# Performance work log

Measured on AMD Instinct MI355X. Metric: run time of the kernel, lower is better.

## Reference

```python
import jax, jax.numpy as jnp
import numpy as np

BN_EPS = 1e-5
LEAKY_SLOPE = 0.2


def setup_inputs() -> dict:
    key = jax.random.key(0)
    k1, k2 = jax.random.split(key, 2)
    B, C, N, O, K = 8, 64, 4096, 64, 20
    x = jax.random.normal(k1, (B, C, N), dtype=jnp.float32)
    W = jax.random.normal(k2, (O, 2 * C), dtype=jnp.float32) * 0.05  # 1x1 conv weight
    gamma = jnp.ones((O,), dtype=jnp.float32)
    beta = jnp.zeros((O,), dtype=jnp.float32)
    return {"x": x, "W": W, "gamma": gamma, "beta": beta, "k": K}


def reference(x, W, gamma, beta, k):
    # x: (B, C, N)
    xt = jnp.transpose(x, (0, 2, 1))  # (B, N, C)
    # kNN via squared euclidean distances (same ordering as cdist p=2)
    sq = jnp.sum(xt * xt, axis=-1)  # (B, N)
    d2 = sq[:, :, None] + sq[:, None, :] - 2.0 * jnp.einsum('bnc,bmc->bnm', xt, xt)
    idx = jax.lax.top_k(-d2, k)[1]  # (B, N, k) nearest neighbors (incl. self)
    # gather neighbor features: (B, N, k, C)
    xj = jax.vmap(lambda f, i: f[i])(xt, idx)
    xi = xt[:, :, None, :]  # (B, N, 1, C)
    edge = jnp.concatenate([xj - xi, jnp.broadcast_to(xi, xj.shape)], axis=-1)  # (B, N, k, 2C)
    # 1x1 conv == channel GEMM
    h = jnp.einsum('bnkc,oc->bnko', edge, W)  # (B, N, k, O)
    # BatchNorm2d, training-mode batch statistics over (B, N, k) per channel
    mean = jnp.mean(h, axis=(0, 1, 2))
    var = jnp.mean(jnp.square(h - mean), axis=(0, 1, 2))
    hn = (h - mean) * jax.lax.rsqrt(var + BN_EPS) * gamma + beta
    # LeakyReLU(0.2); dropout omitted (eval / identity)
    act = jnp.where(hn >= 0, hn, LEAKY_SLOPE * hn)
    # max over the k neighbors -> (B, N, O) -> (B, O, N)
    out = jnp.max(act, axis=2)
    return jnp.transpose(out, (0, 2, 1))
```

## Files before the change

### kernel.cpp

```cpp
#include <hip/hip_runtime.h>
#include <math.h>

#define Bn 8
#define Cc 64
#define Nn 4096
#define Oo 64
#define Kk 20
#define Kh 10
#define QCAP 16
#define NTOT (Bn*Nn*Kk)

typedef __attribute__((ext_vector_type(8))) short short8;
typedef __attribute__((ext_vector_type(4))) float f32x4;

__device__ __forceinline__ unsigned bf16_rn(float v) {
  unsigned u = __float_as_uint(v);
  return (u + 0x7FFFu + ((u >> 16) & 1)) >> 16;
}

__global__ __launch_bounds__(256) void k_split(const float* __restrict__ x,
                                               unsigned short* __restrict__ xs3,
                                               float* __restrict__ sqv) {
  __shared__ float xs[64][68];
  int tid = threadIdx.x;
  int b = blockIdx.x & 7;
  int n0 = (blockIdx.x >> 3) << 6;
  for (int i = 0; i < 4; i++) {
    int c = i * 16 + (tid >> 4);
    int n = (tid & 15) * 4;
    float4 v = *(const float4*)&x[((size_t)b * Cc + c) * Nn + n0 + n];
    *(float4*)&xs[c][n] = v;
  }
  __syncthreads();
  for (int i = 0; i < 4; i++) {
    int n = i * 16 + (tid >> 4);
    int c = (tid & 15) * 4;
    ushort4 h4, m4, l4;
    unsigned short* hp = (unsigned short*)&h4;
    unsigned short* mp = (unsigned short*)&m4;
    unsigned short* lp = (unsigned short*)&l4;
#pragma unroll
    for (int j = 0; j < 4; j++) {
      float v = xs[c + j][n];
      unsigned hb = bf16_rn(v);
      float hf = __uint_as_float(hb << 16);
      float r1 = v - hf;
      unsigned mb = bf16_rn(r1);
      float mf = __uint_as_float(mb << 16);
      float r2 = r1 - mf;
      unsigned lb = bf16_rn(r2);
      hp[j] = (unsigned short)hb;
      mp[j] = (unsigned short)mb;
      lp[j] = (unsigned short)lb;
    }
    size_t o = ((size_t)(b << 12) + n0 + n) * 192 + c;
    *(ushort4*)&xs3[o] = h4;
    *(ushort4*)&xs3[o + 64] = m4;
    *(ushort4*)&xs3[o + 128] = l4;
  }
  if (tid < 64) {
    float s = 0.f;
#pragma unroll
    for (int c = 0; c < 64; c++) { float v = xs[c][tid]; s = fmaf(v, v, s); }
    sqv[b * Nn + n0 + tid] = s;
  }
}

__global__ __launch_bounds__(256) void k_y1z(const float* __restrict__ x,
                                             const float* __restrict__ Wm,
                                             float* __restrict__ y1,
                                             float* __restrict__ z) {
  __shared__ float xs[64][68];
  __shared__ float Wl[64][129];
  int tid = threadIdx.x;
  int b = blockIdx.x & 7;
  int n0 = (blockIdx.x >> 3) << 6;
  for (int i = tid; i < 64 * 128; i += 256) Wl[i >> 7][i & 127] = Wm[i];
  for (int i = 0; i < 4; i++) {
    int c = i * 16 + (tid >> 4);
    int n = (tid & 15) * 4;
    float4 v = *(const float4*)&x[((size_t)b * Cc + c) * Nn + n0 + n];
    *(float4*)&xs[c][n] = v;
  }
  __syncthreads();
  int o = tid & 63, ng = tid >> 6;
  for (int p = 0; p < 4; p++) {
    int nb = p * 16 + ng * 4;
    float a1[4] = {0.f, 0.f, 0.f, 0.f};
    float a2[4] = {0.f, 0.f, 0.f, 0.f};
#pragma unroll 8
    for (int c = 0; c < 64; c++) {
      float4 xv = *(const float4*)&xs[c][nb];
      float w1v = Wl[o][c], w2v = Wl[o][64 + c];
      float xa[4] = {xv.x, xv.y, xv.z, xv.w};
#pragma unroll
      for (int j = 0; j < 4; j++) {
        a1[j] = fmaf(xa[j], w1v, a1[j]);
        a2[j] = fmaf(xa[j], w2v, a2[j]);
      }
    }
#pragma unroll
    for (int j = 0; j < 4; j++) {
      size_t off = ((size_t)b * Nn + n0 + nb + j) * 64 + o;
      y1[off] = a1[j];
      z[off] = a2[j] - a1[j];
    }
  }
}

__global__ __launch_bounds__(256, 4) void k_knn(const unsigned short* __restrict__ xs3,
                                                const float* __restrict__ sqv,
                                                int* __restrict__ idxout) {
  __shared__ alignas(16) short Bs[3][64][72];
  __shared__ float thrS[64];
  __shared__ float sqs[64];
  __shared__ alignas(16) float qk[64][20];
  __shared__ alignas(16) unsigned short qm[64][24];
  __shared__ int qcnt[64];

  const int tid = threadIdx.x;
  const int lane = tid & 63;
  const int w = tid >> 6;
  const int b = blockIdx.x & 7;
  const int n0 = (blockIdx.x >> 3) << 6;
  const int lm = lane & 15;
  const int q = lane >> 4;
  const bool handler = (lane < 32);
  const int hrow = w * 16 + (lane >> 1);
  const bool isL = (lane & 1) == 0;

  float hk[Kh];
  int hix[Kh];
#pragma unroll
  for (int kk = 0; kk < Kh; kk++) { hk[kk] = INFINITY; hix[kk] = 0; }

  if (handler && !isL) { thrS[hrow] = INFINITY; qcnt[hrow] = 0; }

  const size_t arow = ((size_t)(b << 12) + n0 + w * 16 + lm) * 192;
  short8 ah0 = *(const short8*)&xs3[arow + q * 8];
  short8 ah1 = *(const short8*)&xs3[arow + 32 + q * 8];
  short8 am0 = *(const short8*)&xs3[arow + 64 + q * 8];
  short8 am1 = *(const short8*)&xs3[arow + 96 + q * 8];
  short8 al0 = *(const short8*)&xs3[arow + 128 + q * 8];
  short8 al1 = *(const short8*)&xs3[arow + 160 + q * 8];

  const unsigned short* gp = xs3 + (size_t)(b << 12) * 192 + tid * 8;
  short* ld[6];
#pragma unroll
  for (int i = 0; i < 6; i++) {
    int f = i * 256 + tid;
    int r = f / 24;
    int rem = f - r * 24;
    int layer = rem >> 3;
    int qq = rem & 7;
    ld[i] = &Bs[layer][r][qq * 8];
  }

  f32x4 acc[4];

  for (int m0 = 0; m0 < Nn; m0 += 64) {
    __syncthreads();
#pragma unroll
    for (int i = 0; i < 6; i++) {
      short8 v = *(const short8*)(gp + i * 2048);
      *(short8*)ld[i] = v;
    }
    gp += 12288;
    if (tid < 16) ((float4*)sqs)[tid] = ((const float4*)(sqv + b * Nn + m0))[tid];
    __syncthreads();

#pragma unroll
    for (int g = 0; g < 4; g++) {
      const int mr = g * 16 + lm;
      short8 bh0 = *(const short8*)&Bs[0][mr][q * 8];
      short8 bh1 = *(const short8*)&Bs[0][mr][32 + q * 8];
      short8 bm0 = *(const short8*)&Bs[1][mr][q * 8];
      short8 bm1 = *(const short8*)&Bs[1][mr][32 + q * 8];
      short8 bl0 = *(const short8*)&Bs[2][mr][q * 8];
      short8 bl1 = *(const short8*)&Bs[2][mr][32 + q * 8];
      f32x4 a = (f32x4){0.f, 0.f, 0.f, 0.f};
      a = __builtin_amdgcn_mfma_f32_16x16x32_bf16(am0, bm0, a, 0, 0, 0);
      a = __builtin_amdgcn_mfma_f32_16x16x32_bf16(am1, bm1, a, 0, 0, 0);
      a = __builtin_amdgcn_mfma_f32_16x16x32_bf16(ah0, bl0, a, 0, 0, 0);
      a = __builtin_amdgcn_mfma_f32_16x16x32_bf16(ah1, bl1, a, 0, 0, 0);
      a = __builtin_amdgcn_mfma_f32_16x16x32_bf16(al0, bh0, a, 0, 0, 0);
      a = __builtin_amdgcn_mfma_f32_16x16x32_bf16(al1, bh1, a, 0, 0, 0);
      a = __builtin_amdgcn_mfma_f32_16x16x32_bf16(ah0, bm0, a, 0, 0, 0);
      a = __builtin_amdgcn_mfma_f32_16x16x32_bf16(ah1, bm1, a, 0, 0, 0);
      a = __builtin_amdgcn_mfma_f32_16x16x32_bf16(am0, bh0, a, 0, 0, 0);
      a = __builtin_amdgcn_mfma_f32_16x16x32_bf16(am1, bh1, a, 0, 0, 0);
      a = __builtin_amdgcn_mfma_f32_16x16x32_bf16(ah0, bh0, a, 0, 0, 0);
      a = __builtin_amdgcn_mfma_f32_16x16x32_bf16(ah1, bh1, a, 0, 0, 0);
      acc[g] = a;
    }

    unsigned pend = 0;
    {
      float tl[4];
#pragma unroll
      for (int r = 0; r < 4; r++) tl[r] = thrS[w * 16 + q * 4 + r];
#pragma unroll
      for (int g = 0; g < 4; g++) {
        float sv = sqs[g * 16 + lm];
#pragma unroll
        for (int r = 0; r < 4; r++) {
          float key = fmaf(-2.f, acc[g][r], sv);
          acc[g][r] = key;
          if (key < tl[r]) pend |= 1u << (g * 4 + r);
        }
      }
    }

    for (;;) {
      if (pend) {
#pragma unroll
        for (int g = 0; g < 4; g++) {
#pragma unroll
          for (int r = 0; r < 4; r++) {
            unsigned bit = 1u << (g * 4 + r);
            if (pend & bit) {
              int row = w * 16 + q * 4 + r;
              int p = atomicAdd(&qcnt[row], 1);
              if (p < QCAP) {
                qk[row][p] = acc[g][r];
                qm[row][p] = (unsigned short)(m0 + g * 16 + lm);
                pend &= ~bit;
              }
            }
          }
        }
      }
      unsigned long long anyovf = __ballot(pend != 0);

      if (handler) {
        int cn = qcnt[hrow];
        if (cn > QCAP) cn = QCAP;
        for (int p0 = 0; p0 < cn; p0 += 4) {
          float4 kv4 = *(const float4*)&qk[hrow][p0];
          ushort4 mv4 = *(const ushort4*)&qm[hrow][p0];
          float kva[4] = {kv4.x, kv4.y, kv4.z, kv4.w};
          unsigned short mva[4] = {mv4.x, mv4.y, mv4.z, mv4.w};
#pragma unroll
          for (int j = 0; j < 4; j++) {
            bool valid = (p0 + j < cn);
            float kv = kva[j];
            int ki = (int)mva[j];
            bool lins = kv < hk[Kh - 1];
            float pv = lins ? hk[Kh - 1] : kv;
            int pi = lins ? hix[Kh - 1] : ki;
            float rv = __shfl_xor(pv, 1);
            int ri = __shfl_xor(pi, 1);
            float mval = isL ? kv : rv;
            int midx = isL ? ki : ri;
            if (valid && mval < hk[Kh - 1]) {
              bool cm[Kh];
#pragma unroll
              for (int kk = 0; kk < Kh; kk++) cm[kk] = mval < hk[kk];
#pragma unroll
              for (int kk = Kh - 1; kk >= 1; kk--) {
                hk[kk]  = cm[kk] ? (cm[kk - 1] ? hk[kk - 1]  : mval) : hk[kk];
                hix[kk] = cm[kk] ? (cm[kk - 1] ? hix[kk - 1] : midx) : hix[kk];
              }
              if (cm[0]) { hk[0] = mval; hix[0] = midx; }
            }
          }
        }
        if (cn && !isL) { qcnt[hrow] = 0; thrS[hrow] = hk[Kh - 1]; }
      }
      if (!anyovf) break;
      if (pend) {
        float tl[4];
#pragma unroll
        for (int r = 0; r < 4; r++) tl[r] = thrS[w * 16 + q * 4 + r];
#pragma unroll
        for (int g = 0; g < 4; g++)
#pragma unroll
          for (int r = 0; r < 4; r++) {
            unsigned bit = 1u << (g * 4 + r);
            if ((pend & bit) && acc[g][r] >= tl[r]) pend &= ~bit;
          }
      }
    }
  }

  if (handler) {
    size_t base = ((size_t)b * Nn + n0 + hrow) * Kk + (isL ? 0 : Kh);
#pragma unroll
    for (int kk = 0; kk < Kh; kk++) idxout[base + kk] = hix[kk];
  }
}

__global__ __launch_bounds__(256) void k_stats(const float* __restrict__ y1,
                                               const float* __restrict__ z,
                                               const int* __restrict__ idxp,
                                               float* __restrict__ parts) {
  __shared__ float rs[4][64];
  __shared__ float rq[4][64];
  int tid = threadIdx.x;
  int o = tid & 63, g = tid >> 6;
  int b = blockIdx.x & 7;
  int n0 = (blockIdx.x >> 3) << 6;
  const float* y1b = y1 + (size_t)b * Nn * 64;
  float s = 0.f, ss = 0.f;
  for (int t = 0; t < 16; t++) {
    int n = n0 + g + t * 4;
    size_t base = (size_t)b * Nn + n;
    float zv = z[base * 64 + o];
    const int* ip = idxp + base * Kk;
#pragma unroll
    for (int k = 0; k < Kk; k++) {
      int j = ip[k];
      float hv = y1b[(size_t)j * 64 + o] + zv;
      s += hv;
      ss = fmaf(hv, hv, ss);
    }
  }
  rs[g][o] = s;
  rq[g][o] = ss;
  __syncthreads();
  if (tid < 64) {
    parts[(size_t)blockIdx.x * 128 + tid] = rs[0][tid] + rs[1][tid] + rs[2][tid] + rs[3][tid];
    parts[(size_t)blockIdx.x * 128 + 64 + tid] = rq[0][tid] + rq[1][tid] + rq[2][tid] + rq[3][tid];
  }
}

__global__ __launch_bounds__(128) void k_reduce(const float* __restrict__ parts,
                                                float* __restrict__ stats) {
  int tid = threadIdx.x;
  float s = 0.f;
  for (int i = 0; i < 512; i += 4) {
    s += parts[(size_t)i * 128 + tid] + parts[(size_t)(i + 1) * 128 + tid] +
         parts[(size_t)(i + 2) * 128 + tid] + parts[(size_t)(i + 3) * 128 + tid];
  }
  stats[tid] = s;
}

__global__ __launch_bounds__(256) void k_out(const float* __restrict__ y1,
                                             const float* __restrict__ z,
                                             const int* __restrict__ idxp,
                                             const float* __restrict__ stats,
                                             const float* __restrict__ gamma,
                                             const float* __restrict__ beta,
                                             float* __restrict__ out) {
  __shared__ float T[64][65];
  int tid = threadIdx.x;
  int lane = tid & 63;
  int w = tid >> 6;
  int b = blockIdx.x & 7;
  int n0 = (blockIdx.x >> 3) << 6;
  int o = lane;
  const float inv = 1.0f / (float)NTOT;
  float mean = stats[o] * inv;
  float var = fmaf(-mean, mean, stats[64 + o] * inv);
  float sc = gamma[o] * rsqrtf(var + 1e-5f);
  float bi = fmaf(-mean, sc, beta[o]);
  const float* y1b = y1 + (size_t)b * Nn * 64;
  for (int t = 0; t < 16; t++) {
    int nl = w + t * 4;
    size_t base = (size_t)b * Nn + n0 + nl;
    float zv = z[base * 64 + o];
    const int* ip = idxp + base * Kk;
    float mv = -INFINITY;
#pragma unroll
    for (int k = 0; k < Kk; k++) {
      int j = ip[k];
      float hv = y1b[(size_t)j * 64 + o] + zv;
      float hn = fmaf(hv, sc, bi);
      float a = (hn >= 0.f) ? hn : 0.2f * hn;
      mv = fmaxf(mv, a);
    }
    T[o][nl] = mv;
  }
  __syncthreads();
  for (int t = 0; t < 16; t++) {
    int oo = w * 16 + t;
    out[((size_t)b * Oo + oo) * Nn + n0 + lane] = T[oo][lane];
  }
}

extern "C" void kernel_launch(void* const* d_in, const int* in_sizes, int n_in,
                              void* d_out, int out_size, void* d_ws, size_t ws_size,
                              hipStream_t stream) {
  const float* x = (const float*)d_in[0];
  const float* W = (const float*)d_in[1];
  const float* gamma = (const float*)d_in[2];
  const float* beta = (const float*)d_in[3];

  char* ws = (char*)d_ws;
  unsigned short* xs3 = (unsigned short*)ws;
  float* y1 = (float*)ws;
  float* z = (float*)(ws + 8388608);
  float* sq = (float*)(ws + 16777216);
  float* stats = (float*)(ws + 16908288);
  int* idx = (int*)(ws + 16908800);
  float* parts = (float*)(ws + 19530240);
  float* out = (float*)d_out;

  k_split<<<Bn * (Nn / 64), 256, 0, stream>>>(x, xs3, sq);
  k_knn<<<Bn * (Nn / 64), 256, 0, stream>>>(xs3, sq, idx);
  k_y1z<<<Bn * (Nn / 64), 256, 0, stream>>>(x, W, y1, z);
  k_stats<<<Bn * (Nn / 64), 256, 0, stream>>>(y1, z, idx, parts);
  k_reduce<<<1, 128, 0, stream>>>(parts, stats);
  k_out<<<Bn * (Nn / 64), 256, 0, stream>>>(y1, z, idx, stats, gamma, beta, out);
}
```

Before: 403.5 us.

## Split kNN candidate scan across two wave groups and merge top-k

The kNN block grows to 512 threads as two 4-wave groups. Each group scans half of the candidate points with its own shared tiles, queues and thresholds, then group 1 writes its partial top-k to shared memory and group 0 merges it before writing indices. This aims to shorten the per-block serial loop over 4096 candidates and raise parallelism, since grid size stays at 512 blocks. In exchange it doubles LDS use per block, which may reduce occupancy, and each group's pruning thresholds tighten more slowly because it sees only half the points.

```diff
diff --git a/kernel.cpp b/kernel.cpp
--- a/kernel.cpp
+++ b/kernel.cpp
@@ -108,25 +108,28 @@
   }
 }
 
-__global__ __launch_bounds__(256, 4) void k_knn(const unsigned short* __restrict__ xs3,
+__global__ __launch_bounds__(512, 4) void k_knn(const unsigned short* __restrict__ xs3,
                                                 const float* __restrict__ sqv,
                                                 int* __restrict__ idxout) {
-  __shared__ alignas(16) short Bs[3][64][72];
-  __shared__ float thrS[64];
-  __shared__ float sqs[64];
-  __shared__ alignas(16) float qk[64][20];
-  __shared__ alignas(16) unsigned short qm[64][24];
-  __shared__ int qcnt[64];
+  __shared__ alignas(16) short Bs[2][3][64][72];
+  __shared__ float thrS[2][64];
+  __shared__ float sqs[2][64];
+  __shared__ alignas(16) float qk[2][64][20];
+  __shared__ alignas(16) unsigned short qm[2][64][24];
+  __shared__ int qcnt[2][64];
 
   const int tid = threadIdx.x;
   const int lane = tid & 63;
   const int w = tid >> 6;
+  const int grp = w >> 2;
+  const int wg = w & 3;
+  const int tig = tid & 255;
   const int b = blockIdx.x & 7;
   const int n0 = (blockIdx.x >> 3) << 6;
   const int lm = lane & 15;
   const int q = lane >> 4;
   const bool handler = (lane < 32);
-  const int hrow = w * 16 + (lane >> 1);
+  const int hrow = wg * 16 + (lane >> 1);
   const bool isL = (lane & 1) == 0;
 
   float hk[Kh];
@@ -134,9 +137,9 @@
 #pragma unroll
   for (int kk = 0; kk < Kh; kk++) { hk[kk] = INFINITY; hix[kk] = 0; }
 
-  if (handler && !isL) { thrS[hrow] = INFINITY; qcnt[hrow] = 0; }
-
-  const size_t arow = ((size_t)(b << 12) + n0 + w * 16 + lm) * 192;
+  if (handler && !isL) { thrS[grp][hrow] = INFINITY; qcnt[grp][hrow] = 0; }
+
+  const size_t arow = ((size_t)(b << 12) + n0 + wg * 16 + lm) * 192;
   short8 ah0 = *(const short8*)&xs3[arow + q * 8];
   short8 ah1 = *(const short8*)&xs3[arow + 32 + q * 8];
   short8 am0 = *(const short8*)&xs3[arow + 64 + q * 8];
@@ -144,21 +147,22 @@
   short8 al0 = *(const short8*)&xs3[arow + 128 + q * 8];
   short8 al1 = *(const short8*)&xs3[arow + 160 + q * 8];
 
-  const unsigned short* gp = xs3 + (size_t)(b << 12) * 192 + tid * 8;
+  const unsigned short* gp = xs3 + ((size_t)(b << 12) + grp * 2048) * 192 + tig * 8;
   short* ld[6];
 #pragma unroll
   for (int i = 0; i < 6; i++) {
-    int f = i * 256 + tid;
+    int f = i * 256 + tig;
     int r = f / 24;
     int rem = f - r * 24;
     int layer = rem >> 3;
     int qq = rem & 7;
-    ld[i] = &Bs[layer][r][qq * 8];
+    ld[i] = &Bs[grp][layer][r][qq * 8];
   }
 
   f32x4 acc[4];
 
-  for (int m0 = 0; m0 < Nn; m0 += 64) {
+  for (int t = 0; t < 32; t++) {
+    const int m0 = grp * 2048 + t * 64;
     __syncthreads();
 #pragma unroll
     for (int i = 0; i < 6; i++) {
@@ -166,18 +170,18 @@
       *(short8*)ld[i] = v;
     }
     gp += 12288;
-    if (tid < 16) ((float4*)sqs)[tid] = ((const float4*)(sqv + b * Nn + m0))[tid];
+    if (tig < 16) ((float4*)sqs[grp])[tig] = ((const float4*)(sqv + b * Nn + m0))[tig];
     __syncthreads();
 
 #pragma unroll
     for (int g = 0; g < 4; g++) {
       const int mr = g * 16 + lm;
-      short8 bh0 = *(const short8*)&Bs[0][mr][q * 8];
-      short8 bh1 = *(const short8*)&Bs[0][mr][32 + q * 8];
-      short8 bm0 = *(const short8*)&Bs[1][mr][q * 8];
-      short8 bm1 = *(const short8*)&Bs[1][mr][32 + q * 8];
-      short8 bl0 = *(const short8*)&Bs[2][mr][q * 8];
-      short8 bl1 = *(const short8*)&Bs[2][mr][32 + q * 8];
+      short8 bh0 = *(const short8*)&Bs[grp][0][mr][q * 8];
+      short8 bh1 = *(const short8*)&Bs[grp][0][mr][32 + q * 8];
+      short8 bm0 = *(const short8*)&Bs[grp][1][mr][q * 8];
+      short8 bm1 = *(const short8*)&Bs[grp][1][mr][32 + q * 8];
+      short8 bl0 = *(const short8*)&Bs[grp][2][mr][q * 8];
+      short8 bl1 = *(const short8*)&Bs[grp][2][mr][32 + q * 8];
       f32x4 a = (f32x4){0.f, 0.f, 0.f, 0.f};
       a = __builtin_amdgcn_mfma_f32_16x16x32_bf16(am0, bm0, a, 0, 0, 0);
       a = __builtin_amdgcn_mfma_f32_16x16x32_bf16(am1, bm1, a, 0, 0, 0);
@@ -198,10 +202,10 @@
     {
       float tl[4];
 #pragma unroll
-      for (int r = 0; r < 4; r++) tl[r] = thrS[w * 16 + q * 4 + r];
+      for (int r = 0; r < 4; r++) tl[r] = thrS[grp][wg * 16 + q * 4 + r];
 #pragma unroll
       for (int g = 0; g < 4; g++) {
-        float sv = sqs[g * 16 + lm];
+        float sv = sqs[grp][g * 16 + lm];
 #pragma unroll
         for (int r = 0; r < 4; r++) {
           float key = fmaf(-2.f, acc[g][r], sv);
@@ -219,11 +223,11 @@
           for (int r = 0; r < 4; r++) {
             unsigned bit = 1u << (g * 4 + r);
             if (pend & bit) {
-              int row = w * 16 + q * 4 + r;
-              int p = atomicAdd(&qcnt[row], 1);
+              int row = wg * 16 + q * 4 + r;
+              int p = atomicAdd(&qcnt[grp][row], 1);
               if (p < QCAP) {
-                qk[row][p] = acc[g][r];
-                qm[row][p] = (unsigned short)(m0 + g * 16 + lm);
+                qk[grp][row][p] = acc[g][r];
+                qm[grp][row][p] = (unsigned short)(m0 + g * 16 + lm);
                 pend &= ~bit;
               }
             }
@@ -233,11 +237,11 @@
       unsigned long long anyovf = __ballot(pend != 0);
 
       if (handler) {
-        int cn = qcnt[hrow];
+        int cn = qcnt[grp][hrow];
         if (cn > QCAP) cn = QCAP;
         for (int p0 = 0; p0 < cn; p0 += 4) {
-          float4 kv4 = *(const float4*)&qk[hrow][p0];
-          ushort4 mv4 = *(const ushort4*)&qm[hrow][p0];
+          float4 kv4 = *(const float4*)&qk[grp][hrow][p0];
+          ushort4 mv4 = *(const ushort4*)&qm[grp][hrow][p0];
           float kva[4] = {kv4.x, kv4.y, kv4.z, kv4.w};
           unsigned short mva[4] = {mv4.x, mv4.y, mv4.z, mv4.w};
 #pragma unroll
@@ -265,13 +269,13 @@
             }
           }
         }
-        if (cn && !isL) { qcnt[hrow] = 0; thrS[hrow] = hk[Kh - 1]; }
+        if (cn && !isL) { qcnt[grp][hrow] = 0; thrS[grp][hrow] = hk[Kh - 1]; }
       }
       if (!anyovf) break;
       if (pend) {
         float tl[4];
 #pragma unroll
-        for (int r = 0; r < 4; r++) tl[r] = thrS[w * 16 + q * 4 + r];
+        for (int r = 0; r < 4; r++) tl[r] = thrS[grp][wg * 16 + q * 4 + r];
 #pragma unroll
         for (int g = 0; g < 4; g++)
 #pragma unroll
@@ -283,10 +287,48 @@
     }
   }
 
-  if (handler) {
-    size_t base = ((size_t)b * Nn + n0 + hrow) * Kk + (isL ? 0 : Kh);
-#pragma unroll
-    for (int kk = 0; kk < Kh; kk++) idxout[base + kk] = hix[kk];
+  if (grp == 1 && handler) {
+    int base = isL ? 0 : Kh;
+#pragma unroll
+    for (int kk = 0; kk < Kh; kk++) {
+      qk[1][hrow][base + kk] = hk[kk];
+      qm[1][hrow][base + kk] = (unsigned short)hix[kk];
+    }
+  }
+  __syncthreads();
+  if (grp == 0 && handler) {
+    for (int p0 = 0; p0 < Kk; p0 += 4) {
+      float4 kv4 = *(const float4*)&qk[1][hrow][p0];
+      ushort4 mv4 = *(const ushort4*)&qm[1][hrow][p0];
+      float kva[4] = {kv4.x, kv4.y, kv4.z, kv4.w};
+      unsigned short mva[4] = {mv4.x, mv4.y, mv4.z, mv4.w};
+#pragma unroll
+      for (int j = 0; j < 4; j++) {
+        float kv = kva[j];
+        int ki = (int)mva[j];
+        bool lins = kv < hk[Kh - 1];
+        float pv = lins ? hk[Kh - 1] : kv;
+        int pi = lins ? hix[Kh - 1] : ki;
+        float rv = __shfl_xor(pv, 1);
+        int ri = __shfl_xor(pi, 1);
+        float mval = isL ? kv : rv;
+        int midx = isL ? ki : ri;
+        if (mval < hk[Kh - 1]) {
+          bool cm[Kh];
+#pragma unroll
+          for (int kk = 0; kk < Kh; kk++) cm[kk] = mval < hk[kk];
+#pragma unroll
+          for (int kk = Kh - 1; kk >= 1; kk--) {
+            hk[kk]  = cm[kk] ? (cm[kk - 1] ? hk[kk - 1]  : mval) : hk[kk];
+            hix[kk] = cm[kk] ? (cm[kk - 1] ? hix[kk - 1] : midx) : hix[kk];
+          }
+          if (cm[0]) { hk[0] = mval; hix[0] = midx; }
+        }
+      }
+    }
+    size_t obase = ((size_t)b * Nn + n0 + hrow) * Kk + (isL ? 0 : Kh);
+#pragma unroll
+    for (int kk = 0; kk < Kh; kk++) idxout[obase + kk] = hix[kk];
   }
 }
 
@@ -397,7 +439,7 @@
   float* out = (float*)d_out;
 
   k_split<<<Bn * (Nn / 64), 256, 0, stream>>>(x, xs3, sq);
-  k_knn<<<Bn * (Nn / 64), 256, 0, stream>>>(xs3, sq, idx);
+  k_knn<<<Bn * (Nn / 64), 512, 0, stream>>>(xs3, sq, idx);
   k_y1z<<<Bn * (Nn / 64), 256, 0, stream>>>(x, W, y1, z);
   k_stats<<<Bn * (Nn / 64), 256, 0, stream>>>(y1, z, idx, parts);
   k_reduce<<<1, 128, 0, stream>>>(parts, stats);
```

Result: faster. 384.3 us (-4.8%).
